# Kernel tuning notes

Measured on AMD Instinct MI355X. Metric: run time of the kernel, lower is better.

## Reference

```python
import jax, jax.numpy as jnp
import numpy as np
from jax import lax

DIM = 256
NUM_HEADS = 8
HEAD_DIM = DIM // NUM_HEADS  # 32
TOPK = 4
SCALE = 2  # spatial upscale factor between upper_feat grid and x grid


def conv1x1(x, W, b):
    # x: [B,Cin,H,W], W: [Cout,Cin], b: [Cout]
    return jnp.einsum('bchw,oc->bohw', x, W) + b[None, :, None, None]


def setup_inputs() -> dict:
    key = jax.random.key(0)
    ks = jax.random.split(key, 12)
    f32 = jnp.float32
    B, C, H, W = 2, DIM, 64, 64
    Hu, Wu = H // 2, W // 2
    s = 0.05
    return {
        'x': jax.random.normal(ks[0], (B, C, H, W), f32),
        'upper_feat': jax.random.normal(ks[1], (B, C, Hu, Wu), f32),
        # q: Conv(dim, all_head_dim, 1) with BN folded -> weight + bias
        'Wq': jax.random.normal(ks[2], (DIM, DIM), f32) * s,
        'bq': jnp.zeros((DIM,), f32),
        # kv: Conv(dim, 2*all_head_dim, 1)
        'Wkv': jax.random.normal(ks[3], (2 * DIM, DIM), f32) * s,
        'bkv': jnp.zeros((2 * DIM,), f32),
        # proj: Conv(all_head_dim, dim, 1)
        'Wproj': jax.random.normal(ks[4], (DIM, DIM), f32) * s,
        'bproj': jnp.zeros((DIM,), f32),
        # pe: depthwise 7x7 conv, groups=dim -> weight [dim,1,7,7]
        'Wpe': jax.random.normal(ks[5], (DIM, 1, 7, 7), f32) * s,
        'bpe': jnp.zeros((DIM,), f32),
        # gate_conv1d: Conv1d(2*head_dim, head_dim, 1) -> [head_dim, 2*head_dim]
        'Wg': jax.random.normal(ks[6], (HEAD_DIM, 2 * HEAD_DIM), f32) * s,
        'bg': jnp.zeros((HEAD_DIM,), f32),
    }


def reference(x, upper_feat, Wq, bq, Wkv, bkv, Wproj, bproj, Wpe, bpe, Wg, bg):
    B, C, H, W = x.shape
    N = H * W
    Hu, Wu = upper_feat.shape[2], upper_feat.shape[3]
    Nu = Hu * Wu
    nh, hd = NUM_HEADS, HEAD_DIM

    # queries from lower feature, keys/values from upper feature
    q = conv1x1(x, Wq, bq).reshape(B, nh, hd, N).transpose(0, 1, 3, 2)        # [B,h,N,hd]
    kv = conv1x1(upper_feat, Wkv, bkv).reshape(B, nh, 2 * hd, Nu).transpose(0, 1, 3, 2)
    k, v = kv[..., :hd], kv[..., hd:]                                         # [B,h,Nu,hd]

    sim = jnp.einsum('bhnd,bhmd->bhnm', q, k) * (hd ** -0.5)                  # [B,h,N,Nu]
    attn = jax.nn.softmax(sim, axis=-1)
    coarse_out = jnp.einsum('bhnm,bhmd->bhnd', attn, v)                       # [B,h,N,hd]

    # fine path: gumbel top-k selection over upper grid, gather 2x2 blocks from x grid
    f_kv = conv1x1(x, Wkv, bkv).reshape(B, nh, 2 * hd, N).transpose(0, 1, 3, 2)
    f_k, f_v = f_kv[..., :hd], f_kv[..., hd:]                                 # [B,h,N,hd]

    global_sim = sim.mean(axis=2)                                             # [B,h,Nu]
    gumbel = jax.random.gumbel(jax.random.key(42), global_sim.shape, global_sim.dtype)
    soft_weights = jax.nn.softmax(global_sim + gumbel, axis=-1)
    _, topk_idx = lax.top_k(soft_weights, TOPK)                               # [B,h,topk]

    h_idx = (topk_idx // Wu) * SCALE
    w_idx = (topk_idx % Wu) * SCALE
    idx = jnp.concatenate(
        [(h_idx + dh) * W + (w_idx + dw) for dh in range(SCALE) for dw in range(SCALE)],
        axis=-1,
    )                                                                          # [B,h,4*topk]

    topk_k = jnp.take_along_axis(f_k, idx[..., None], axis=2)                 # [B,h,4*topk,hd]
    topk_v = jnp.take_along_axis(f_v, idx[..., None], axis=2)

    fine_attn = jax.nn.softmax(jnp.einsum('bhnd,bhmd->bhnm', q, topk_k) * (hd ** -0.5), axis=-1)
    refined_out = jnp.einsum('bhnm,bhmd->bhnd', fine_attn, topk_v)            # [B,h,N,hd]

    fusion = jnp.concatenate([coarse_out, refined_out], axis=-1)              # [B,h,N,2hd]
    gate = jax.nn.sigmoid(jnp.einsum('bhnc,dc->bhnd', fusion, Wg) + bg)       # [B,h,N,hd]
    out = gate * refined_out + (1.0 - gate) * coarse_out

    out = out.transpose(0, 1, 3, 2).reshape(B, C, H, W)

    # positional encoding path: depthwise 7x7 conv on v, bilinear upsample
    v_r = v.transpose(0, 1, 3, 2).reshape(B, C, Hu, Wu)
    v_pe = lax.conv_general_dilated(
        v_r, Wpe, window_strides=(1, 1), padding=((3, 3), (3, 3)),
        dimension_numbers=('NCHW', 'OIHW', 'NCHW'), feature_group_count=C,
    ) + bpe[None, :, None, None]
    v_pe = jax.image.resize(v_pe, (B, C, H, W), method='bilinear')

    return conv1x1(out + v_pe, Wproj, bproj)
```

## Files before the change

kernel.cpp:

```cpp
#include <hip/hip_runtime.h>
#include <hip/hip_bf16.h>
#include <math.h>
#include <stdint.h>

#define NB   2
#define NC   256
#define NSP  4096
#define NUSP 1024
#define NHEADS 8
#define HDIM 32
constexpr float SCL  = 0.17677669529663687f;
constexpr float QSCL = 0.17677669529663687f * 1.4426950408889634f;

typedef short short8 __attribute__((ext_vector_type(8)));
typedef float f32x4  __attribute__((ext_vector_type(4)));

__device__ __forceinline__ float fexp2(float x) {
#if __has_builtin(__builtin_amdgcn_exp2f)
  return __builtin_amdgcn_exp2f(x);
#else
  return exp2f(x);
#endif
}

__device__ __align__(16) float g_kv    [NB * 512 * NUSP];
__device__ __align__(16) float g_qm    [NB * NHEADS * HDIM];
__device__ __align__(16) float g_vpe   [NB * NC * NSP];
__device__ __align__(16) short g_qbf   [NB * NHEADS * NSP * HDIM];
__device__ __align__(16) short g_kbf   [NB * NHEADS * NUSP * HDIM];
__device__ __align__(16) short g_vbf   [NB * NHEADS * HDIM * NUSP];
__device__ __align__(16) short g_tkKbf [NB * NHEADS * 16 * 32];
__device__ __align__(16) short g_tkVT  [NB * NHEADS * 32 * 32];
__device__ __align__(16) short g_xT    [NB * NSP * 256];
__device__ __align__(16) short g_uT    [NB * NUSP * 256];
__device__ __align__(16) short g_sumT  [NB * NSP * 256];
__device__ __align__(16) short g_wbf   [262144];
__device__ __align__(16) short g_wgbf  [2048];

__device__ __forceinline__ short f2bf(float f) {
  return (short)((__float_as_uint(f) + 0x8000u) >> 16);
}

__device__ __forceinline__ void threefry2x32_042(uint32_t x0, uint32_t x1,
                                                 uint32_t& r0, uint32_t& r1) {
  const uint32_t ks0 = 0u, ks1 = 42u, ks2 = 0u ^ 42u ^ 0x1BD11BDAu;
  x0 += ks0; x1 += ks1;
#define TFR(R) { x0 += x1; x1 = (x1 << (R)) | (x1 >> (32 - (R))); x1 ^= x0; }
  TFR(13) TFR(15) TFR(26) TFR(6)  x0 += ks1; x1 += ks2 + 1u;
  TFR(17) TFR(29) TFR(16) TFR(24) x0 += ks2; x1 += ks0 + 2u;
  TFR(13) TFR(15) TFR(26) TFR(6)  x0 += ks0; x1 += ks1 + 3u;
  TFR(17) TFR(29) TFR(16) TFR(24) x0 += ks1; x1 += ks2 + 4u;
  TFR(13) TFR(15) TFR(26) TFR(6)  x0 += ks2; x1 += ks0 + 5u;
#undef TFR
  r0 = x0; r1 = x1;
}

__device__ __forceinline__ float gumbel_at(uint32_t i) {
  uint32_t y0, y1;
  threefry2x32_042(0u, i, y0, y1);
  uint32_t bits = y0 ^ y1;
  uint32_t fb = (bits >> 9) | 0x3f800000u;
  float u = __uint_as_float(fb) - 1.0f;
  u = fmaxf(u, 1.17549435e-38f);
  return -logf(-logf(u));
}

__global__ __launch_bounds__(256) void k_pack_in(const float* __restrict__ x,
                                                 const float* __restrict__ upper,
                                                 const float* __restrict__ Wq,
                                                 const float* __restrict__ Wkv,
                                                 const float* __restrict__ Wproj,
                                                 const float* __restrict__ Wg) {
  const int sec = blockIdx.x;
  const int tid = threadIdx.x;
  if (sec < 160) {
    __shared__ float Ls[32][65];
    const float* src;
    short* dst;
    int b, n0, Nsp;
    if (sec < 128) { b = sec >> 6; n0 = (sec & 63) * 64; Nsp = NSP;
                     src = x + (size_t)b * 256 * NSP;  dst = g_xT + (size_t)b * NSP * 256; }
    else           { int s2 = sec - 128; b = s2 >> 4; n0 = (s2 & 15) * 64; Nsp = NUSP;
                     src = upper + (size_t)b * 256 * NUSP; dst = g_uT + (size_t)b * NUSP * 256; }
    for (int cc = 0; cc < 8; cc++) {
      __syncthreads();
      for (int i = tid; i < 2048; i += 256) {
        int d = i >> 6, nl = i & 63;
        Ls[d][nl] = src[(size_t)(cc * 32 + d) * Nsp + n0 + nl];
      }
      __syncthreads();
      int nl = tid >> 2, dseg = (tid & 3) * 8;
      short8 v;
      #pragma unroll
      for (int j = 0; j < 8; j++) v[j] = f2bf(Ls[dseg + j][nl]);
      *(short8*)&dst[(size_t)(n0 + nl) * 256 + cc * 32 + dseg] = v;
    }
  } else {
    if (sec == 160) {
      for (int i = tid; i < 512; i += 256) g_qm[i] = 0.f;
      #pragma unroll
      for (int j = 0; j < 8; j++) g_wgbf[tid * 8 + j] = f2bf(Wg[tid * 8 + j]);
    }
    int base = (sec - 160) * 8192 + tid * 32;
    const float* s;
    if (base < 65536)       s = Wq + base;
    else if (base < 196608) s = Wkv + (base - 65536);
    else                    s = Wproj + (base - 196608);
    short* d = g_wbf + base;
    #pragma unroll
    for (int j = 0; j < 8; j++) {
      float4 f = *(const float4*)&s[j * 4];
      d[j*4+0] = f2bf(f.x); d[j*4+1] = f2bf(f.y);
      d[j*4+2] = f2bf(f.z); d[j*4+3] = f2bf(f.w);
    }
  }
}

__device__ __forceinline__ void gemm_mfma(const short* __restrict__ Wbf,
                                          const short* __restrict__ ST,
                                          int b, int o0, int n0, int Nsp,
                                          int w, int col, int quad,
                                          f32x4 acc[4]) {
  const short* wrow = Wbf + (size_t)(o0 + w * 16 + col) * 256 + quad * 8;
  const short* srow = ST + ((size_t)b * Nsp + n0 + col) * 256 + quad * 8;
  #pragma unroll
  for (int kc = 0; kc < 8; kc++) {
    short8 af = *(const short8*)&wrow[kc * 32];
    #pragma unroll
    for (int t = 0; t < 4; t++) {
      short8 bf = *(const short8*)&srow[(size_t)(t * 16) * 256 + kc * 32];
      acc[t] = __builtin_amdgcn_mfma_f32_16x16x32_bf16(af, bf, acc[t], 0, 0, 0);
    }
  }
}

__global__ __launch_bounds__(256) void k_gemms(const float* __restrict__ bq,
                                               const float* __restrict__ bkv) {
  __shared__ float Ls[64][65];
  const int bx = blockIdx.x;
  const int tid = threadIdx.x;
  const int lane = tid & 63, w = tid >> 6, col = lane & 15, quad = lane >> 4;
  f32x4 acc[4] = {{0,0,0,0},{0,0,0,0},{0,0,0,0},{0,0,0,0}};

  if (bx < 512) {
    const int b = bx >> 8, o0 = ((bx >> 6) & 3) * 64, n0 = (bx & 63) * 64;
    gemm_mfma(g_wbf, g_xT, b, o0, n0, NSP, w, col, quad, acc);
    float sums[4];
    #pragma unroll
    for (int r = 0; r < 4; r++) {
      int ol = w * 16 + quad * 4 + r;
      float bv = bq[o0 + ol];
      float s = 0.f;
      #pragma unroll
      for (int t = 0; t < 4; t++) {
        float val = acc[t][r] + bv;
        Ls[ol][t * 16 + col] = val;
        s += val;
      }
      sums[r] = s;
    }
    #pragma unroll
    for (int st = 1; st < 16; st <<= 1)
      #pragma unroll
      for (int r = 0; r < 4; r++) sums[r] += __shfl_xor(sums[r], st, 64);
    if (col == 0) {
      #pragma unroll
      for (int r = 0; r < 4; r++)
        atomicAdd(&g_qm[b * 256 + o0 + w * 16 + quad * 4 + r], sums[r] * (1.0f / 4096.0f));
    }
    __syncthreads();
    int nl = tid >> 2, dseg = (tid & 3) * 8;
    #pragma unroll
    for (int hh = 0; hh < 2; hh++) {
      short8 v;
      #pragma unroll
      for (int j = 0; j < 8; j++) v[j] = f2bf(Ls[hh * 32 + dseg + j][nl] * QSCL);
      int bh = b * 8 + ((o0 + hh * 32) >> 5);
      *(short8*)&g_qbf[((size_t)bh * NSP + n0 + nl) * 32 + dseg] = v;
    }
  } else {
    const int idx = bx - 512;
    const int b = idx >> 7, o0 = ((idx >> 4) & 7) * 64, n0 = (idx & 15) * 64;
    gemm_mfma(g_wbf + 65536, g_uT, b, o0, n0, NUSP, w, col, quad, acc);
    #pragma unroll
    for (int r = 0; r < 4; r++) {
      int ol = w * 16 + quad * 4 + r;
      float bv = bkv[o0 + ol];
      float* orow = g_kv + ((size_t)b * 512 + o0 + ol) * NUSP + n0;
      #pragma unroll
      for (int t = 0; t < 4; t++) {
        float val = acc[t][r] + bv;
        orow[t * 16 + col] = val;
        Ls[ol][t * 16 + col] = val;
      }
    }
    __syncthreads();
    const int bh = b * 8 + (o0 >> 6);
    {
      int m = tid >> 2, dseg = (tid & 3) * 8;
      short8 v;
      #pragma unroll
      for (int j = 0; j < 8; j++) v[j] = f2bf(Ls[dseg + j][m]);
      *(short8*)&g_kbf[((size_t)bh * NUSP + n0 + m) * 32 + dseg] = v;
    }
    {
      int d = tid >> 3, m8 = (tid & 7) * 8;
      short8 v;
      #pragma unroll
      for (int j = 0; j < 8; j++) v[j] = f2bf(Ls[32 + d][m8 + j]);
      *(short8*)&g_vbf[((size_t)bh * 32 + d) * NUSP + n0 + m8] = v;
    }
  }
}

union MidSmem {
  struct {
    float zbuf[1024]; float qml[32]; float rv[256]; int ri[256];
    int chosen[4]; int pos[16]; float xg[16][256]; float wl[64][65];
  } t;
  struct {
    float src[32][33]; float pl[32][33]; float wk[49];
  } v;
};

__global__ __launch_bounds__(256) void k_mid(const float* __restrict__ x,
                                             const float* __restrict__ Wkv,
                                             const float* __restrict__ bkv,
                                             const float* __restrict__ Wpe,
                                             const float* __restrict__ bpe) {
  __shared__ MidSmem sm;
  const int tid = threadIdx.x;
  if (blockIdx.x < 16) {
    const int bh = blockIdx.x;
    const int b = bh >> 3, h = bh & 7;
    if (tid < 32) sm.t.qml[tid] = g_qm[bh * 32 + tid];
    __syncthreads();
    const float* kbase = g_kv + ((size_t)b * 512 + h * 64) * NUSP;
    float zv[4];
    #pragma unroll
    for (int r = 0; r < 4; r++) {
      int m = r * 256 + tid;
      float dot = 0.f;
      #pragma unroll 8
      for (int d = 0; d < 32; d++) dot += sm.t.qml[d] * kbase[(size_t)d * NUSP + m];
      float z = dot * SCL + gumbel_at((uint32_t)(bh * 1024 + m));
      zv[r] = z; sm.t.zbuf[m] = z;
    }
    __syncthreads();
    float mx = fmaxf(fmaxf(zv[0], zv[1]), fmaxf(zv[2], zv[3]));
    sm.t.rv[tid] = mx; __syncthreads();
    for (int st = 128; st > 0; st >>= 1) {
      if (tid < st) sm.t.rv[tid] = fmaxf(sm.t.rv[tid], sm.t.rv[tid + st]);
      __syncthreads();
    }
    float zmax = sm.t.rv[0]; __syncthreads();
    float sp = 0.f; float ev[4];
    #pragma unroll
    for (int r = 0; r < 4; r++) { ev[r] = __expf(zv[r] - zmax); sp += ev[r]; }
    sm.t.rv[tid] = sp; __syncthreads();
    for (int st = 128; st > 0; st >>= 1) {
      if (tid < st) sm.t.rv[tid] += sm.t.rv[tid + st];
      __syncthreads();
    }
    float ssum = sm.t.rv[0]; __syncthreads();
    #pragma unroll
    for (int r = 0; r < 4; r++) sm.t.zbuf[r * 256 + tid] = ev[r] / ssum;
    __syncthreads();
    for (int t = 0; t < 4; t++) {
      float bv = -2.0f; int bi = 0;
      #pragma unroll
      for (int r = 0; r < 4; r++) {
        int m = r * 256 + tid;
        float v = sm.t.zbuf[m];
        if (v > bv) { bv = v; bi = m; }
      }
      sm.t.rv[tid] = bv; sm.t.ri[tid] = bi; __syncthreads();
      for (int st = 128; st > 0; st >>= 1) {
        if (tid < st) {
          float v2 = sm.t.rv[tid + st]; int i2 = sm.t.ri[tid + st];
          if (v2 > sm.t.rv[tid] || (v2 == sm.t.rv[tid] && i2 < sm.t.ri[tid])) {
            sm.t.rv[tid] = v2; sm.t.ri[tid] = i2;
          }
        }
        __syncthreads();
      }
      if (tid == 0) { sm.t.chosen[t] = sm.t.ri[0]; sm.t.zbuf[sm.t.ri[0]] = -2.0f; }
      __syncthreads();
    }
    if (tid < 16) {
      int t = tid & 3, g2 = tid >> 2;
      int dh = g2 >> 1, dw = g2 & 1;
      int m = sm.t.chosen[t];
      int hi = (m >> 5) * 2 + dh, wi = (m & 31) * 2 + dw;
      sm.t.pos[g2 * 4 + t] = hi * 64 + wi;
    }
    __syncthreads();
    for (int i = tid; i < 16 * 256; i += 256) {
      int j = i >> 8, c = i & 255;
      sm.t.xg[j][c] = x[((size_t)b * 256 + c) * NSP + sm.t.pos[j]];
    }
    const int dd = tid & 63, jg = tid >> 6;
    const float bia = bkv[h * 64 + dd];
    float a4[4] = {bia, bia, bia, bia};
    for (int cc2 = 0; cc2 < 4; cc2++) {
      __syncthreads();
      for (int i = tid; i < 4096; i += 256) {
        int r = i >> 6, c = i & 63;
        sm.t.wl[r][c] = Wkv[(size_t)(h * 64 + r) * 256 + cc2 * 64 + c];
      }
      __syncthreads();
      #pragma unroll
      for (int jj = 0; jj < 4; jj++) {
        int j = jg * 4 + jj;
        float a = 0.f;
        #pragma unroll 8
        for (int c = 0; c < 64; c++) a += sm.t.xg[j][cc2 * 64 + c] * sm.t.wl[dd][c];
        a4[jj] += a;
      }
    }
    #pragma unroll
    for (int jj = 0; jj < 4; jj++) {
      int j = jg * 4 + jj;
      if (dd < 32) {
        g_tkKbf[((size_t)bh * 16 + j) * 32 + dd] = f2bf(a4[jj]);
      } else {
        int d = dd - 32;
        g_tkVT[((size_t)bh * 32 + d) * 32 + j] = f2bf(a4[jj]);
        g_tkVT[((size_t)bh * 32 + d) * 32 + 16 + j] = 0;
      }
    }
  } else {
    const int idx = blockIdx.x - 16;
    const int c = idx & 255, b = idx >> 8;
    const int h = c >> 5, d = c & 31;
    const float* vrow = g_kv + ((size_t)b * 512 + h * 64 + 32 + d) * NUSP;
    for (int i = tid; i < 1024; i += 256) sm.v.src[i >> 5][i & 31] = vrow[i];
    if (tid < 49) sm.v.wk[tid] = Wpe[c * 49 + tid];
    __syncthreads();
    const float bia = bpe[c];
    for (int i = tid; i < 1024; i += 256) {
      int hu = i >> 5, wu = i & 31;
      float s = bia;
      #pragma unroll
      for (int kh = 0; kh < 7; kh++) {
        int ih = hu + kh - 3;
        if (ih < 0 || ih > 31) continue;
        #pragma unroll
        for (int kw = 0; kw < 7; kw++) {
          int iw = wu + kw - 3;
          if (iw < 0 || iw > 31) continue;
          s += sm.v.src[ih][iw] * sm.v.wk[kh * 7 + kw];
        }
      }
      sm.v.pl[hu][wu] = s;
    }
    __syncthreads();
    float* orow = g_vpe + ((size_t)b * 256 + c) * NSP;
    for (int i = tid; i < 4096; i += 256) {
      int hh = i >> 6, ww = i & 63;
      int ih = hh >> 1, iw = ww >> 1;
      int ih2 = (hh & 1) ? min(ih + 1, 31) : max(ih - 1, 0);
      int iw2 = (ww & 1) ? min(iw + 1, 31) : max(iw - 1, 0);
      float a  = 0.75f * sm.v.pl[ih][iw]  + 0.25f * sm.v.pl[ih][iw2];
      float bb = 0.75f * sm.v.pl[ih2][iw] + 0.25f * sm.v.pl[ih2][iw2];
      orow[i] = 0.75f * a + 0.25f * bb;
    }
  }
}

__global__ __launch_bounds__(256) void k_flash(const float* __restrict__ bg) {
  const int bh = blockIdx.y;
  const int b = bh >> 3, h = bh & 7;
  const int tid = threadIdx.x;
  const int lane = tid & 63;
  const int w = tid >> 6;
  const int col = lane & 15;
  const int quad = lane >> 4;
  const int n0 = blockIdx.x * 128 + w * 32;

  __shared__ short Ps[8][16][88];
  short* PsA = &Ps[w * 2][0][0];
  short* PsB = &Ps[w * 2 + 1][0][0];

  const short* kb = g_kbf + (size_t)bh * NUSP * 32;
  const short* vb = g_vbf + (size_t)bh * 32 * NUSP;

  short8 qfA = *(const short8*)&g_qbf[((size_t)bh * NSP + n0 + col) * 32 + quad * 8];
  short8 qfB = *(const short8*)&g_qbf[((size_t)bh * NSP + n0 + 16 + col) * 32 + quad * 8];

  f32x4 oA0 = {0,0,0,0}, oA1 = {0,0,0,0}, oB0 = {0,0,0,0}, oB1 = {0,0,0,0};
  float lA[4] = {0,0,0,0}, lB[4] = {0,0,0,0};

  for (int kt = 0; kt < 16; kt++) {
    short8 kf[4];
    #pragma unroll
    for (int t = 0; t < 4; t++)
      kf[t] = *(const short8*)&kb[((size_t)(kt * 64 + t * 16 + col)) * 32 + quad * 8];
    f32x4 sA[4], sB[4];
    #pragma unroll
    for (int t = 0; t < 4; t++) {
      f32x4 z = {0,0,0,0};
      sA[t] = __builtin_amdgcn_mfma_f32_16x16x32_bf16(qfA, kf[t], z, 0, 0, 0);
      sB[t] = __builtin_amdgcn_mfma_f32_16x16x32_bf16(qfB, kf[t], z, 0, 0, 0);
    }
    #pragma unroll
    for (int t = 0; t < 4; t++)
      #pragma unroll
      for (int r = 0; r < 4; r++) {
        float pA = fexp2(sA[t][r]);
        float pB = fexp2(sB[t][r]);
        sA[t][r] = pA; lA[r] += pA;
        sB[t][r] = pB; lB[r] += pB;
      }
    #pragma unroll
    for (int t = 0; t < 4; t++)
      #pragma unroll
      for (int r = 0; r < 4; r++) {
        PsA[(quad * 4 + r) * 88 + t * 16 + col] = f2bf(sA[t][r]);
        PsB[(quad * 4 + r) * 88 + t * 16 + col] = f2bf(sB[t][r]);
      }
    short8 vf0 = *(const short8*)&vb[(size_t)col * NUSP + kt * 64 + quad * 8];
    short8 vf1 = *(const short8*)&vb[(size_t)(col + 16) * NUSP + kt * 64 + quad * 8];
    short8 vf2 = *(const short8*)&vb[(size_t)col * NUSP + kt * 64 + 32 + quad * 8];
    short8 vf3 = *(const short8*)&vb[(size_t)(col + 16) * NUSP + kt * 64 + 32 + quad * 8];
    short8 pA0 = *(const short8*)&PsA[col * 88 + quad * 8];
    short8 pA1 = *(const short8*)&PsA[col * 88 + 32 + quad * 8];
    short8 pB0 = *(const short8*)&PsB[col * 88 + quad * 8];
    short8 pB1 = *(const short8*)&PsB[col * 88 + 32 + quad * 8];
    oA0 = __builtin_amdgcn_mfma_f32_16x16x32_bf16(pA0, vf0, oA0, 0, 0, 0);
    oB0 = __builtin_amdgcn_mfma_f32_16x16x32_bf16(pB0, vf0, oB0, 0, 0, 0);
    oA1 = __builtin_amdgcn_mfma_f32_16x16x32_bf16(pA0, vf1, oA1, 0, 0, 0);
    oB1 = __builtin_amdgcn_mfma_f32_16x16x32_bf16(pB0, vf1, oB1, 0, 0, 0);
    oA0 = __builtin_amdgcn_mfma_f32_16x16x32_bf16(pA1, vf2, oA0, 0, 0, 0);
    oB0 = __builtin_amdgcn_mfma_f32_16x16x32_bf16(pB1, vf2, oB0, 0, 0, 0);
    oA1 = __builtin_amdgcn_mfma_f32_16x16x32_bf16(pA1, vf3, oA1, 0, 0, 0);
    oB1 = __builtin_amdgcn_mfma_f32_16x16x32_bf16(pB1, vf3, oB1, 0, 0, 0);
  }
  #pragma unroll
  for (int st = 1; st < 16; st <<= 1)
    #pragma unroll
    for (int r = 0; r < 4; r++) {
      lA[r] += __shfl_xor(lA[r], st, 64);
      lB[r] += __shfl_xor(lB[r], st, 64);
    }

  const float bg0 = bg[col], bg1 = bg[col + 16];
  short8 kff = *(const short8*)&g_tkKbf[(size_t)bh * 512 + col * 32 + quad * 8];
  short8 vt0 = *(const short8*)&g_tkVT[(size_t)bh * 1024 + col * 32 + quad * 8];
  short8 vt1 = *(const short8*)&g_tkVT[(size_t)bh * 1024 + (col + 16) * 32 + quad * 8];
  short8 b1a = *(const short8*)&g_wgbf[col * 64 + quad * 8];
  short8 b1b = *(const short8*)&g_wgbf[col * 64 + 32 + quad * 8];
  short8 b2a = *(const short8*)&g_wgbf[(col + 16) * 64 + quad * 8];
  short8 b2b = *(const short8*)&g_wgbf[(col + 16) * 64 + 32 + quad * 8];

  #pragma unroll
  for (int tt = 0; tt < 2; tt++) {
    const int nt = n0 + tt * 16;
    short8 qf = tt ? qfB : qfA;
    f32x4 o0 = tt ? oB0 : oA0;
    f32x4 o1 = tt ? oB1 : oA1;
    float* lr = tt ? lB : lA;
    short* myPs = tt ? PsB : PsA;
    f32x4 zf = {0,0,0,0};
    f32x4 co0, co1;
    #pragma unroll
    for (int r = 0; r < 4; r++) {
      float inv = 1.0f / lr[r];
      co0[r] = o0[r] * inv;
      co1[r] = o1[r] * inv;
    }
    f32x4 sf = __builtin_amdgcn_mfma_f32_16x16x32_bf16(qf, kff, zf, 0, 0, 0);
    float fl[4];
    #pragma unroll
    for (int r = 0; r < 4; r++) { float p = fexp2(sf[r]); sf[r] = p; fl[r] = p; }
    #pragma unroll
    for (int st = 1; st < 16; st <<= 1)
      #pragma unroll
      for (int r = 0; r < 4; r++) fl[r] += __shfl_xor(fl[r], st, 64);
    #pragma unroll
    for (int r = 0; r < 4; r++)
      myPs[(quad * 4 + r) * 88 + col] = f2bf(sf[r]);
    short8 pff = {0, 0, 0, 0, 0, 0, 0, 0};
    if (quad < 2) pff = *(const short8*)&myPs[col * 88 + quad * 8];
    f32x4 rf0 = __builtin_amdgcn_mfma_f32_16x16x32_bf16(pff, vt0, zf, 0, 0, 0);
    f32x4 rf1 = __builtin_amdgcn_mfma_f32_16x16x32_bf16(pff, vt1, zf, 0, 0, 0);
    #pragma unroll
    for (int r = 0; r < 4; r++) {
      float inv = 1.0f / fl[r];
      rf0[r] *= inv; rf1[r] *= inv;
    }
    #pragma unroll
    for (int r = 0; r < 4; r++) {
      int q = quad * 4 + r;
      myPs[q * 88 + col]      = f2bf(co0[r]);
      myPs[q * 88 + col + 16] = f2bf(co1[r]);
      myPs[q * 88 + col + 32] = f2bf(rf0[r]);
      myPs[q * 88 + col + 48] = f2bf(rf1[r]);
    }
    short8 a1 = *(const short8*)&myPs[col * 88 + quad * 8];
    short8 a2 = *(const short8*)&myPs[col * 88 + 32 + quad * 8];
    f32x4 G0 = __builtin_amdgcn_mfma_f32_16x16x32_bf16(a1, b1a, zf, 0, 0, 0);
    G0 = __builtin_amdgcn_mfma_f32_16x16x32_bf16(a2, b1b, G0, 0, 0, 0);
    f32x4 G1 = __builtin_amdgcn_mfma_f32_16x16x32_bf16(a1, b2a, zf, 0, 0, 0);
    G1 = __builtin_amdgcn_mfma_f32_16x16x32_bf16(a2, b2b, G1, 0, 0, 0);
    const float* vpe0 = g_vpe + ((size_t)(b * 256 + h * 32 + col)) * NSP + nt;
    const float* vpe1 = g_vpe + ((size_t)(b * 256 + h * 32 + col + 16)) * NSP + nt;
    short* dstb = g_sumT + ((size_t)b * NSP + nt) * 256 + h * 32;
    #pragma unroll
    for (int r = 0; r < 4; r++) {
      int q = quad * 4 + r;
      float g0 = 1.0f / (1.0f + __expf(-(G0[r] + bg0)));
      float g1 = 1.0f / (1.0f + __expf(-(G1[r] + bg1)));
      float out0 = g0 * rf0[r] + (1.0f - g0) * co0[r] + vpe0[q];
      float out1 = g1 * rf1[r] + (1.0f - g1) * co1[r] + vpe1[q];
      dstb[(size_t)q * 256 + col]      = f2bf(out0);
      dstb[(size_t)q * 256 + col + 16] = f2bf(out1);
    }
  }
}

__global__ __launch_bounds__(256) void k_gemm_proj(const float* __restrict__ bias,
                                                   float* __restrict__ out) {
  const int b = blockIdx.z;
  const int o0 = blockIdx.y * 64;
  const int n0 = blockIdx.x * 64;
  const int tid = threadIdx.x;
  const int lane = tid & 63, w = tid >> 6, col = lane & 15, quad = lane >> 4;
  f32x4 acc[4] = {{0,0,0,0},{0,0,0,0},{0,0,0,0},{0,0,0,0}};
  gemm_mfma(g_wbf + 196608, g_sumT, b, o0, n0, NSP, w, col, quad, acc);
  #pragma unroll
  for (int r = 0; r < 4; r++) {
    int o = o0 + w * 16 + quad * 4 + r;
    float bv = bias[o];
    float* orow = out + ((size_t)b * 256 + o) * NSP + n0;
    #pragma unroll
    for (int t = 0; t < 4; t++)
      orow[t * 16 + col] = acc[t][r] + bv;
  }
}

extern "C" void kernel_launch(void* const* d_in, const int* in_sizes, int n_in,
                              void* d_out, int out_size, void* d_ws, size_t ws_size,
                              hipStream_t stream) {
  const float* x     = (const float*)d_in[0];
  const float* upper = (const float*)d_in[1];
  const float* Wq    = (const float*)d_in[2];
  const float* bq    = (const float*)d_in[3];
  const float* Wkv   = (const float*)d_in[4];
  const float* bkv   = (const float*)d_in[5];
  const float* Wproj = (const float*)d_in[6];
  const float* bproj = (const float*)d_in[7];
  const float* Wpe   = (const float*)d_in[8];
  const float* bpe   = (const float*)d_in[9];
  const float* Wg    = (const float*)d_in[10];
  const float* bg    = (const float*)d_in[11];
  float* out = (float*)d_out;
  (void)d_ws; (void)ws_size; (void)in_sizes; (void)n_in; (void)out_size;

  k_pack_in<<<dim3(192), dim3(256), 0, stream>>>(x, upper, Wq, Wkv, Wproj, Wg);
  k_gemms<<<dim3(768), dim3(256), 0, stream>>>(bq, bkv);
  k_mid<<<dim3(528), dim3(256), 0, stream>>>(x, Wkv, bkv, Wpe, bpe);
  k_flash<<<dim3(32, 16), dim3(256), 0, stream>>>(bg);
  k_gemm_proj<<<dim3(64, 4, 2), dim3(256), 0, stream>>>(bproj, out);
}
```

Measured before the change: 208.5 us.

## Fuse five kernels into one cooperative persistent kernel with grid syncs

Replaces the five separate launches (pack, gemms, mid, flash, proj) with one cooperative kernel of 512 blocks that runs each phase in turn, separated by grid-wide syncs and sharing a union of shared-memory layouts. The aim is to remove per-launch overhead and the gaps between kernels. In exchange, the larger shared-memory union and the occupancy hint of 2 blocks per CU may limit residency. Phases with more work units than blocks now loop, and every block must wait at each grid barrier.

```diff
diff --git a/kernel.cpp b/kernel.cpp
--- a/kernel.cpp
+++ b/kernel.cpp
@@ -1,7 +1,10 @@
 #include <hip/hip_runtime.h>
+#include <hip/hip_cooperative_groups.h>
 #include <hip/hip_bf16.h>
 #include <math.h>
 #include <stdint.h>
+
+namespace cg = cooperative_groups;
 
 #define NB   2
 #define NC   256
@@ -65,16 +68,23 @@
   return -logf(-logf(u));
 }
 
-__global__ __launch_bounds__(256) void k_pack_in(const float* __restrict__ x,
-                                                 const float* __restrict__ upper,
-                                                 const float* __restrict__ Wq,
-                                                 const float* __restrict__ Wkv,
-                                                 const float* __restrict__ Wproj,
-                                                 const float* __restrict__ Wg) {
-  const int sec = blockIdx.x;
+union MegaSmem {
+  struct { float Ls[32][65]; } pack;
+  struct { float Ls[64][65]; } gemm;
+  struct {
+    float zbuf[1024]; float qml[32]; float rv[256]; int ri[256];
+    int chosen[4]; int pos[16]; float xg[16][256]; float wl[64][65];
+  } t;
+  struct { float src[32][33]; float pl[32][33]; float wk[49]; } v;
+  struct { short Ps[8][16][88]; } fl;
+};
+
+__device__ void ph_pack(MegaSmem* sm, int sec,
+                        const float* __restrict__ x, const float* __restrict__ upper,
+                        const float* __restrict__ Wq, const float* __restrict__ Wkv,
+                        const float* __restrict__ Wproj, const float* __restrict__ Wg) {
   const int tid = threadIdx.x;
   if (sec < 160) {
-    __shared__ float Ls[32][65];
     const float* src;
     short* dst;
     int b, n0, Nsp;
@@ -86,13 +96,13 @@
       __syncthreads();
       for (int i = tid; i < 2048; i += 256) {
         int d = i >> 6, nl = i & 63;
-        Ls[d][nl] = src[(size_t)(cc * 32 + d) * Nsp + n0 + nl];
+        sm->pack.Ls[d][nl] = src[(size_t)(cc * 32 + d) * Nsp + n0 + nl];
       }
       __syncthreads();
       int nl = tid >> 2, dseg = (tid & 3) * 8;
       short8 v;
       #pragma unroll
-      for (int j = 0; j < 8; j++) v[j] = f2bf(Ls[dseg + j][nl]);
+      for (int j = 0; j < 8; j++) v[j] = f2bf(sm->pack.Ls[dseg + j][nl]);
       *(short8*)&dst[(size_t)(n0 + nl) * 256 + cc * 32 + dseg] = v;
     }
   } else {
@@ -134,10 +144,9 @@
   }
 }
 
-__global__ __launch_bounds__(256) void k_gemms(const float* __restrict__ bq,
-                                               const float* __restrict__ bkv) {
-  __shared__ float Ls[64][65];
-  const int bx = blockIdx.x;
+__device__ void ph_gemm(MegaSmem* sm, int bx,
+                        const float* __restrict__ bq, const float* __restrict__ bkv) {
+  __syncthreads();
   const int tid = threadIdx.x;
   const int lane = tid & 63, w = tid >> 6, col = lane & 15, quad = lane >> 4;
   f32x4 acc[4] = {{0,0,0,0},{0,0,0,0},{0,0,0,0},{0,0,0,0}};
@@ -154,7 +163,7 @@
       #pragma unroll
       for (int t = 0; t < 4; t++) {
         float val = acc[t][r] + bv;
-        Ls[ol][t * 16 + col] = val;
+        sm->gemm.Ls[ol][t * 16 + col] = val;
         s += val;
       }
       sums[r] = s;
@@ -174,7 +183,7 @@
     for (int hh = 0; hh < 2; hh++) {
       short8 v;
       #pragma unroll
-      for (int j = 0; j < 8; j++) v[j] = f2bf(Ls[hh * 32 + dseg + j][nl] * QSCL);
+      for (int j = 0; j < 8; j++) v[j] = f2bf(sm->gemm.Ls[hh * 32 + dseg + j][nl] * QSCL);
       int bh = b * 8 + ((o0 + hh * 32) >> 5);
       *(short8*)&g_qbf[((size_t)bh * NSP + n0 + nl) * 32 + dseg] = v;
     }
@@ -191,7 +200,7 @@
       for (int t = 0; t < 4; t++) {
         float val = acc[t][r] + bv;
         orow[t * 16 + col] = val;
-        Ls[ol][t * 16 + col] = val;
+        sm->gemm.Ls[ol][t * 16 + col] = val;
       }
     }
     __syncthreads();
@@ -200,40 +209,29 @@
       int m = tid >> 2, dseg = (tid & 3) * 8;
       short8 v;
       #pragma unroll
-      for (int j = 0; j < 8; j++) v[j] = f2bf(Ls[dseg + j][m]);
+      for (int j = 0; j < 8; j++) v[j] = f2bf(sm->gemm.Ls[dseg + j][m]);
       *(short8*)&g_kbf[((size_t)bh * NUSP + n0 + m) * 32 + dseg] = v;
     }
     {
       int d = tid >> 3, m8 = (tid & 7) * 8;
       short8 v;
       #pragma unroll
-      for (int j = 0; j < 8; j++) v[j] = f2bf(Ls[32 + d][m8 + j]);
+      for (int j = 0; j < 8; j++) v[j] = f2bf(sm->gemm.Ls[32 + d][m8 + j]);
       *(short8*)&g_vbf[((size_t)bh * 32 + d) * NUSP + n0 + m8] = v;
     }
   }
 }
 
-union MidSmem {
-  struct {
-    float zbuf[1024]; float qml[32]; float rv[256]; int ri[256];
-    int chosen[4]; int pos[16]; float xg[16][256]; float wl[64][65];
-  } t;
-  struct {
-    float src[32][33]; float pl[32][33]; float wk[49];
-  } v;
-};
-
-__global__ __launch_bounds__(256) void k_mid(const float* __restrict__ x,
-                                             const float* __restrict__ Wkv,
-                                             const float* __restrict__ bkv,
-                                             const float* __restrict__ Wpe,
-                                             const float* __restrict__ bpe) {
-  __shared__ MidSmem sm;
+__device__ void ph_mid(MegaSmem* sm, int u,
+                       const float* __restrict__ x, const float* __restrict__ Wkv,
+                       const float* __restrict__ bkv, const float* __restrict__ Wpe,
+                       const float* __restrict__ bpe) {
+  __syncthreads();
   const int tid = threadIdx.x;
-  if (blockIdx.x < 16) {
-    const int bh = blockIdx.x;
+  if (u < 16) {
+    const int bh = u;
     const int b = bh >> 3, h = bh & 7;
-    if (tid < 32) sm.t.qml[tid] = g_qm[bh * 32 + tid];
+    if (tid < 32) sm->t.qml[tid] = g_qm[bh * 32 + tid];
     __syncthreads();
     const float* kbase = g_kv + ((size_t)b * 512 + h * 64) * NUSP;
     float zv[4];
@@ -242,62 +240,62 @@
       int m = r * 256 + tid;
       float dot = 0.f;
       #pragma unroll 8
-      for (int d = 0; d < 32; d++) dot += sm.t.qml[d] * kbase[(size_t)d * NUSP + m];
+      for (int d = 0; d < 32; d++) dot += sm->t.qml[d] * kbase[(size_t)d * NUSP + m];
       float z = dot * SCL + gumbel_at((uint32_t)(bh * 1024 + m));
-      zv[r] = z; sm.t.zbuf[m] = z;
+      zv[r] = z; sm->t.zbuf[m] = z;
     }
     __syncthreads();
     float mx = fmaxf(fmaxf(zv[0], zv[1]), fmaxf(zv[2], zv[3]));
-    sm.t.rv[tid] = mx; __syncthreads();
+    sm->t.rv[tid] = mx; __syncthreads();
     for (int st = 128; st > 0; st >>= 1) {
-      if (tid < st) sm.t.rv[tid] = fmaxf(sm.t.rv[tid], sm.t.rv[tid + st]);
-      __syncthreads();
-    }
-    float zmax = sm.t.rv[0]; __syncthreads();
+      if (tid < st) sm->t.rv[tid] = fmaxf(sm->t.rv[tid], sm->t.rv[tid + st]);
+      __syncthreads();
+    }
+    float zmax = sm->t.rv[0]; __syncthreads();
     float sp = 0.f; float ev[4];
     #pragma unroll
     for (int r = 0; r < 4; r++) { ev[r] = __expf(zv[r] - zmax); sp += ev[r]; }
-    sm.t.rv[tid] = sp; __syncthreads();
+    sm->t.rv[tid] = sp; __syncthreads();
     for (int st = 128; st > 0; st >>= 1) {
-      if (tid < st) sm.t.rv[tid] += sm.t.rv[tid + st];
-      __syncthreads();
-    }
-    float ssum = sm.t.rv[0]; __syncthreads();
-    #pragma unroll
-    for (int r = 0; r < 4; r++) sm.t.zbuf[r * 256 + tid] = ev[r] / ssum;
+      if (tid < st) sm->t.rv[tid] += sm->t.rv[tid + st];
+      __syncthreads();
+    }
+    float ssum = sm->t.rv[0]; __syncthreads();
+    #pragma unroll
+    for (int r = 0; r < 4; r++) sm->t.zbuf[r * 256 + tid] = ev[r] / ssum;
     __syncthreads();
     for (int t = 0; t < 4; t++) {
       float bv = -2.0f; int bi = 0;
       #pragma unroll
       for (int r = 0; r < 4; r++) {
         int m = r * 256 + tid;
-        float v = sm.t.zbuf[m];
+        float v = sm->t.zbuf[m];
         if (v > bv) { bv = v; bi = m; }
       }
-      sm.t.rv[tid] = bv; sm.t.ri[tid] = bi; __syncthreads();
+      sm->t.rv[tid] = bv; sm->t.ri[tid] = bi; __syncthreads();
       for (int st = 128; st > 0; st >>= 1) {
         if (tid < st) {
-          float v2 = sm.t.rv[tid + st]; int i2 = sm.t.ri[tid + st];
-          if (v2 > sm.t.rv[tid] || (v2 == sm.t.rv[tid] && i2 < sm.t.ri[tid])) {
-            sm.t.rv[tid] = v2; sm.t.ri[tid] = i2;
+          float v2 = sm->t.rv[tid + st]; int i2 = sm->t.ri[tid + st];
+          if (v2 > sm->t.rv[tid] || (v2 == sm->t.rv[tid] && i2 < sm->t.ri[tid])) {
+            sm->t.rv[tid] = v2; sm->t.ri[tid] = i2;
           }
         }
         __syncthreads();
       }
-      if (tid == 0) { sm.t.chosen[t] = sm.t.ri[0]; sm.t.zbuf[sm.t.ri[0]] = -2.0f; }
+      if (tid == 0) { sm->t.chosen[t] = sm->t.ri[0]; sm->t.zbuf[sm->t.ri[0]] = -2.0f; }
       __syncthreads();
     }
     if (tid < 16) {
       int t = tid & 3, g2 = tid >> 2;
       int dh = g2 >> 1, dw = g2 & 1;
-      int m = sm.t.chosen[t];
+      int m = sm->t.chosen[t];
       int hi = (m >> 5) * 2 + dh, wi = (m & 31) * 2 + dw;
-      sm.t.pos[g2 * 4 + t] = hi * 64 + wi;
+      sm->t.pos[g2 * 4 + t] = hi * 64 + wi;
     }
     __syncthreads();
     for (int i = tid; i < 16 * 256; i += 256) {
       int j = i >> 8, c = i & 255;
-      sm.t.xg[j][c] = x[((size_t)b * 256 + c) * NSP + sm.t.pos[j]];
+      sm->t.xg[j][c] = x[((size_t)b * 256 + c) * NSP + sm->t.pos[j]];
     }
     const int dd = tid & 63, jg = tid >> 6;
     const float bia = bkv[h * 64 + dd];
@@ -306,7 +304,7 @@
       __syncthreads();
       for (int i = tid; i < 4096; i += 256) {
         int r = i >> 6, c = i & 63;
-        sm.t.wl[r][c] = Wkv[(size_t)(h * 64 + r) * 256 + cc2 * 64 + c];
+        sm->t.wl[r][c] = Wkv[(size_t)(h * 64 + r) * 256 + cc2 * 64 + c];
       }
       __syncthreads();
       #pragma unroll
@@ -314,7 +312,7 @@
         int j = jg * 4 + jj;
         float a = 0.f;
         #pragma unroll 8
-        for (int c = 0; c < 64; c++) a += sm.t.xg[j][cc2 * 64 + c] * sm.t.wl[dd][c];
+        for (int c = 0; c < 64; c++) a += sm->t.xg[j][cc2 * 64 + c] * sm->t.wl[dd][c];
         a4[jj] += a;
       }
     }
@@ -330,12 +328,12 @@
       }
     }
   } else {
-    const int idx = blockIdx.x - 16;
+    const int idx = u - 16;
     const int c = idx & 255, b = idx >> 8;
     const int h = c >> 5, d = c & 31;
     const float* vrow = g_kv + ((size_t)b * 512 + h * 64 + 32 + d) * NUSP;
-    for (int i = tid; i < 1024; i += 256) sm.v.src[i >> 5][i & 31] = vrow[i];
-    if (tid < 49) sm.v.wk[tid] = Wpe[c * 49 + tid];
+    for (int i = tid; i < 1024; i += 256) sm->v.src[i >> 5][i & 31] = vrow[i];
+    if (tid < 49) sm->v.wk[tid] = Wpe[c * 49 + tid];
     __syncthreads();
     const float bia = bpe[c];
     for (int i = tid; i < 1024; i += 256) {
@@ -349,10 +347,10 @@
         for (int kw = 0; kw < 7; kw++) {
           int iw = wu + kw - 3;
           if (iw < 0 || iw > 31) continue;
-          s += sm.v.src[ih][iw] * sm.v.wk[kh * 7 + kw];
+          s += sm->v.src[ih][iw] * sm->v.wk[kh * 7 + kw];
         }
       }
-      sm.v.pl[hu][wu] = s;
+      sm->v.pl[hu][wu] = s;
     }
     __syncthreads();
     float* orow = g_vpe + ((size_t)b * 256 + c) * NSP;
@@ -361,26 +359,27 @@
       int ih = hh >> 1, iw = ww >> 1;
       int ih2 = (hh & 1) ? min(ih + 1, 31) : max(ih - 1, 0);
       int iw2 = (ww & 1) ? min(iw + 1, 31) : max(iw - 1, 0);
-      float a  = 0.75f * sm.v.pl[ih][iw]  + 0.25f * sm.v.pl[ih][iw2];
-      float bb = 0.75f * sm.v.pl[ih2][iw] + 0.25f * sm.v.pl[ih2][iw2];
+      float a  = 0.75f * sm->v.pl[ih][iw]  + 0.25f * sm->v.pl[ih][iw2];
+      float bb = 0.75f * sm->v.pl[ih2][iw] + 0.25f * sm->v.pl[ih2][iw2];
       orow[i] = 0.75f * a + 0.25f * bb;
     }
   }
 }
 
-__global__ __launch_bounds__(256) void k_flash(const float* __restrict__ bg) {
-  const int bh = blockIdx.y;
+__device__ void ph_flash(MegaSmem* sm, int u, const float* __restrict__ bg) {
+  __syncthreads();
+  const int bh = u >> 5;
   const int b = bh >> 3, h = bh & 7;
+  const int bxx = u & 31;
   const int tid = threadIdx.x;
   const int lane = tid & 63;
   const int w = tid >> 6;
   const int col = lane & 15;
   const int quad = lane >> 4;
-  const int n0 = blockIdx.x * 128 + w * 32;
-
-  __shared__ short Ps[8][16][88];
-  short* PsA = &Ps[w * 2][0][0];
-  short* PsB = &Ps[w * 2 + 1][0][0];
+  const int n0 = bxx * 128 + w * 32;
+
+  short* PsA = &sm->fl.Ps[w * 2][0][0];
+  short* PsB = &sm->fl.Ps[w * 2 + 1][0][0];
 
   const short* kb = g_kbf + (size_t)bh * NUSP * 32;
   const short* vb = g_vbf + (size_t)bh * 32 * NUSP;
@@ -470,13 +469,13 @@
       co1[r] = o1[r] * inv;
     }
     f32x4 sf = __builtin_amdgcn_mfma_f32_16x16x32_bf16(qf, kff, zf, 0, 0, 0);
-    float fl[4];
-    #pragma unroll
-    for (int r = 0; r < 4; r++) { float p = fexp2(sf[r]); sf[r] = p; fl[r] = p; }
+    float flr[4];
+    #pragma unroll
+    for (int r = 0; r < 4; r++) { float p = fexp2(sf[r]); sf[r] = p; flr[r] = p; }
     #pragma unroll
     for (int st = 1; st < 16; st <<= 1)
       #pragma unroll
-      for (int r = 0; r < 4; r++) fl[r] += __shfl_xor(fl[r], st, 64);
+      for (int r = 0; r < 4; r++) flr[r] += __shfl_xor(flr[r], st, 64);
     #pragma unroll
     for (int r = 0; r < 4; r++)
       myPs[(quad * 4 + r) * 88 + col] = f2bf(sf[r]);
@@ -486,7 +485,7 @@
     f32x4 rf1 = __builtin_amdgcn_mfma_f32_16x16x32_bf16(pff, vt1, zf, 0, 0, 0);
     #pragma unroll
     for (int r = 0; r < 4; r++) {
-      float inv = 1.0f / fl[r];
+      float inv = 1.0f / flr[r];
       rf0[r] *= inv; rf1[r] *= inv;
     }
     #pragma unroll
@@ -519,11 +518,10 @@
   }
 }
 
-__global__ __launch_bounds__(256) void k_gemm_proj(const float* __restrict__ bias,
-                                                   float* __restrict__ out) {
-  const int b = blockIdx.z;
-  const int o0 = blockIdx.y * 64;
-  const int n0 = blockIdx.x * 64;
+__device__ void ph_proj(int u, const float* __restrict__ bias, float* __restrict__ out) {
+  const int b = u >> 8;
+  const int o0 = ((u >> 6) & 3) * 64;
+  const int n0 = (u & 63) * 64;
   const int tid = threadIdx.x;
   const int lane = tid & 63, w = tid >> 6, col = lane & 15, quad = lane >> 4;
   f32x4 acc[4] = {{0,0,0,0},{0,0,0,0},{0,0,0,0},{0,0,0,0}};
@@ -537,6 +535,34 @@
     for (int t = 0; t < 4; t++)
       orow[t * 16 + col] = acc[t][r] + bv;
   }
+}
+
+__global__ __launch_bounds__(256, 2) void k_all(const float* __restrict__ x,
+                                                const float* __restrict__ upper,
+                                                const float* __restrict__ Wq,
+                                                const float* __restrict__ bq,
+                                                const float* __restrict__ Wkv,
+                                                const float* __restrict__ bkv,
+                                                const float* __restrict__ Wproj,
+                                                const float* __restrict__ bproj,
+                                                const float* __restrict__ Wpe,
+                                                const float* __restrict__ bpe,
+                                                const float* __restrict__ Wg,
+                                                const float* __restrict__ bg,
+                                                float* __restrict__ out) {
+  __shared__ MegaSmem sm;
+  cg::grid_group grid = cg::this_grid();
+  const int bx = blockIdx.x;
+
+  if (bx < 192) ph_pack(&sm, bx, x, upper, Wq, Wkv, Wproj, Wg);
+  grid.sync();
+  for (int u = bx; u < 768; u += 512) ph_gemm(&sm, u, bq, bkv);
+  grid.sync();
+  for (int u = bx; u < 528; u += 512) ph_mid(&sm, u, x, Wkv, bkv, Wpe, bpe);
+  grid.sync();
+  ph_flash(&sm, bx, bg);
+  grid.sync();
+  ph_proj(bx, bproj, out);
 }
 
 extern "C" void kernel_launch(void* const* d_in, const int* in_sizes, int n_in,
@@ -557,9 +583,10 @@
   float* out = (float*)d_out;
   (void)d_ws; (void)ws_size; (void)in_sizes; (void)n_in; (void)out_size;
 
-  k_pack_in<<<dim3(192), dim3(256), 0, stream>>>(x, upper, Wq, Wkv, Wproj, Wg);
-  k_gemms<<<dim3(768), dim3(256), 0, stream>>>(bq, bkv);
-  k_mid<<<dim3(528), dim3(256), 0, stream>>>(x, Wkv, bkv, Wpe, bpe);
-  k_flash<<<dim3(32, 16), dim3(256), 0, stream>>>(bg);
-  k_gemm_proj<<<dim3(64, 4, 2), dim3(256), 0, stream>>>(bproj, out);
-}
+  void* kargs[] = {
+    (void*)&x, (void*)&upper, (void*)&Wq, (void*)&bq, (void*)&Wkv, (void*)&bkv,
+    (void*)&Wproj, (void*)&bproj, (void*)&Wpe, (void*)&bpe, (void*)&Wg, (void*)&bg,
+    (void*)&out
+  };
+  hipLaunchCooperativeKernel((const void*)k_all, dim3(512), dim3(256), kargs, 0, stream);
+}
```

Measured after the change: 471.6 us. 2.26x slower.
